# Optimization experiments

Hardware: AMD Instinct MI355X
Metric: run time of the kernel (lower is better)

The kernel has to match this reference:

```python
import jax, jax.numpy as jnp
import numpy as np

D_MODEL = 1024
NHEAD = 16
HEAD_DIM = D_MODEL // NHEAD
D_FF = 4096
EPS = 1e-5


def _layer_norm(x, g, b):
    mu = jnp.mean(x, axis=-1, keepdims=True)
    var = jnp.mean((x - mu) ** 2, axis=-1, keepdims=True)
    return (x - mu) * jax.lax.rsqrt(var + EPS) * g + b


def _rotate_every_two(x):
    x1 = x[..., ::2]
    x2 = x[..., 1::2]
    return jnp.stack([-x2, x1], axis=-1).reshape(x.shape)


def _rope_cos_sin(pos_start, length, head_dim, dtype):
    inv_freq = 1.0 / (10000.0 ** (jnp.arange(0, head_dim, 2, dtype=jnp.float32) / head_dim))
    pos = jnp.arange(pos_start, pos_start + length, dtype=jnp.float32)
    ang = jnp.einsum('i,j->ij', pos, inv_freq)  # (len, head_dim/2)
    cos = jnp.repeat(jnp.cos(ang), 2, axis=-1).astype(dtype)
    sin = jnp.repeat(jnp.sin(ang), 2, axis=-1).astype(dtype)
    return cos, sin


def setup_inputs() -> dict:
    key = jax.random.key(0)
    ks = jax.random.split(key, 16)
    s = 1.0 / np.sqrt(D_MODEL)
    sf = 1.0 / np.sqrt(D_FF)
    inp = {
        'src': jax.random.normal(ks[0], (2048, 2, D_MODEL), jnp.float32),
        'src_mask': jnp.ones((2048, 2048), jnp.float32),
        'Wq': jax.random.normal(ks[1], (D_MODEL, D_MODEL), jnp.float32) * s,
        'bq': jnp.zeros((D_MODEL,), jnp.float32),
        'Wk': jax.random.normal(ks[2], (D_MODEL, D_MODEL), jnp.float32) * s,
        'bk': jnp.zeros((D_MODEL,), jnp.float32),
        'Wv': jax.random.normal(ks[3], (D_MODEL, D_MODEL), jnp.float32) * s,
        'bv': jnp.zeros((D_MODEL,), jnp.float32),
        'Wo': jax.random.normal(ks[4], (D_MODEL, D_MODEL), jnp.float32) * s,
        'bo': jnp.zeros((D_MODEL,), jnp.float32),
        'W1': jax.random.normal(ks[5], (D_MODEL, D_FF), jnp.float32) * s,
        'b1': jnp.zeros((D_FF,), jnp.float32),
        'W2': jax.random.normal(ks[6], (D_FF, D_MODEL), jnp.float32) * sf,
        'b2': jnp.zeros((D_MODEL,), jnp.float32),
        'g1': jnp.ones((D_MODEL,), jnp.float32),
        'be1': jnp.zeros((D_MODEL,), jnp.float32),
        'g2': jnp.ones((D_MODEL,), jnp.float32),
        'be2': jnp.zeros((D_MODEL,), jnp.float32),
    }
    return inp


def _attention(q, k, v, attn_mask):
    # q, k, v: (S, B, D) already projected
    s, b, _ = q.shape
    kl = k.shape[0]

    def heads(x):
        # (L, B, D) -> (B, H, L, dh)
        return x.reshape(x.shape[0], b, NHEAD, HEAD_DIM).transpose(1, 2, 0, 3)

    qh, kh, vh = heads(q), heads(k), heads(v)
    q_cos, q_sin = _rope_cos_sin(0, s, HEAD_DIM, qh.dtype)
    k_cos, k_sin = _rope_cos_sin(0, kl, HEAD_DIM, kh.dtype)
    qh = qh * q_cos + _rotate_every_two(qh) * q_sin
    kh = kh * k_cos + _rotate_every_two(kh) * k_sin

    scores = jnp.einsum('bhqd,bhkd->bhqk', qh, kh) / np.sqrt(HEAD_DIM)
    if attn_mask is not None:
        scores = jnp.where(attn_mask[None, None, :, :] < 0.1, -jnp.inf, scores)
    w = jax.nn.softmax(scores, axis=-1)
    out = jnp.einsum('bhqk,bhkd->bhqd', w, vh)  # (B, H, S, dh)
    out = out.transpose(2, 0, 1, 3).reshape(s, b, D_MODEL)
    return out


def reference(src, src_mask, Wq, bq, Wk, bk, Wv, bv, Wo, bo, W1, b1, W2, b2, g1, be1, g2, be2):
    q = src @ Wq + bq
    k = src @ Wk + bk
    v = src @ Wv + bv
    attn = _attention(q, k, v, src_mask) @ Wo + bo
    src2 = _layer_norm(src + attn, g1, be1)
    ff = jax.nn.relu(src2 @ W1 + b1) @ W2 + b2
    out = _layer_norm(src2 + ff, g2, be2)
    return out
```

## Files before the change

kernel.cpp:

```cpp
#include <hip/hip_runtime.h>
#include <math.h>

#define S_LEN 2048
#define DM 1024
#define NH 16
#define HD 64
#define DFF 4096
#define MROWS 4096

typedef unsigned short u16;
typedef __attribute__((ext_vector_type(8))) __bf16 bf16x8;
typedef __attribute__((ext_vector_type(4))) float f32x4;
typedef __attribute__((ext_vector_type(16))) float f32x16;
typedef __attribute__((ext_vector_type(4))) int int32x4;

__device__ __forceinline__ u16 f2bf(float f) {
  unsigned u = __float_as_uint(f);
  unsigned r = (u + 0x7fffu + ((u >> 16) & 1u)) >> 16;
  return (u16)r;
}

__device__ __forceinline__ float bf2f(u16 u) {
  return __uint_as_float((unsigned)u << 16);
}

__device__ __forceinline__ unsigned cvtpk_bf16(float lo, float hi) {
  unsigned r;
  asm("v_cvt_pk_bf16_f32 %0, %1, %2" : "=v"(r) : "v"(lo), "v"(hi));
  return r;
}

__device__ __forceinline__ void gload_lds16(const void* g, void* l) {
  __builtin_amdgcn_global_load_lds((__attribute__((address_space(1))) void*)g,
                                   (__attribute__((address_space(3))) void*)l, 16, 0, 0);
}

__global__ __launch_bounds__(256) void k_transpose4(const float* __restrict__ W0, const float* __restrict__ W1,
                                                    const float* __restrict__ W2, const float* __restrict__ W3,
                                                    u16* __restrict__ T0, u16* __restrict__ T1,
                                                    u16* __restrict__ T2, u16* __restrict__ T3) {
  __shared__ float tile[32][33];
  const float* W = blockIdx.z == 0 ? W0 : blockIdx.z == 1 ? W1 : blockIdx.z == 2 ? W2 : W3;
  u16* Wt = blockIdx.z == 0 ? T0 : blockIdx.z == 1 ? T1 : blockIdx.z == 2 ? T2 : T3;
  int n0 = blockIdx.x * 32, k0 = blockIdx.y * 32;
  int tx = threadIdx.x & 31, ty = threadIdx.x >> 5;
  #pragma unroll
  for (int r = ty; r < 32; r += 8) tile[r][tx] = W[(size_t)(k0 + r) * 1024 + n0 + tx];
  __syncthreads();
  #pragma unroll
  for (int r = ty; r < 32; r += 8) Wt[(size_t)(n0 + r) * 1024 + k0 + tx] = f2bf(tile[tx][r]);
}

__global__ __launch_bounds__(256) void k_transpose_bf16(const float* __restrict__ W,
                                                        u16* __restrict__ Wt, int K, int N) {
  __shared__ float tile[32][33];
  int n0 = blockIdx.x * 32, k0 = blockIdx.y * 32;
  int tx = threadIdx.x & 31, ty = threadIdx.x >> 5;
  #pragma unroll
  for (int r = ty; r < 32; r += 8) tile[r][tx] = W[(size_t)(k0 + r) * N + n0 + tx];
  __syncthreads();
  #pragma unroll
  for (int r = ty; r < 32; r += 8) Wt[(size_t)(n0 + r) * K + k0 + tx] = f2bf(tile[tx][r]);
}

__global__ __launch_bounds__(256) void k_f2bf4(const float4* __restrict__ in,
                                               ushort4* __restrict__ out, int n4) {
  int i = blockIdx.x * 256 + threadIdx.x;
  if (i >= n4) return;
  float4 v = in[i];
  ushort4 o;
  o.x = f2bf(v.x); o.y = f2bf(v.y); o.z = f2bf(v.z); o.w = f2bf(v.w);
  out[i] = o;
}

__global__ __launch_bounds__(256) void k_rope_table(float* __restrict__ cosT,
                                                    float* __restrict__ sinT) {
  int idx = blockIdx.x * 256 + threadIdx.x;
  if (idx >= S_LEN * 32) return;
  int s = idx >> 5, i = idx & 31;
  float inv = powf(10000.f, -(float)(2 * i) / 64.f);
  float ang = (float)s * inv;
  cosT[idx] = cosf(ang);
  sinT[idx] = sinf(ang);
}

__global__ __launch_bounds__(256) void k_cat3(const float* __restrict__ a, const float* __restrict__ b,
                                              const float* __restrict__ c, float* __restrict__ o) {
  int i = blockIdx.x * 256 + threadIdx.x;
  if (i >= 3072) return;
  o[i] = i < 1024 ? a[i] : (i < 2048 ? b[i - 1024] : c[i - 2048]);
}

__global__ __launch_bounds__(256) void k_mask_flags(const float* __restrict__ mask,
                                                    unsigned char* __restrict__ flags) {
  int kt = blockIdx.x, qt = blockIdx.y;
  const float* mp = mask + (size_t)(qt * 64) * S_LEN + kt * 64;
  int tr = threadIdx.x >> 2;
  int tc = (threadIdx.x & 3) * 16;
  int ok = 1;
  #pragma unroll
  for (int c = 0; c < 16; c += 4) {
    float4 v = *(const float4*)(mp + (size_t)tr * S_LEN + tc + c);
    ok &= (v.x >= 0.1f) & (v.y >= 0.1f) & (v.z >= 0.1f) & (v.w >= 0.1f);
  }
  ok = __all(ok) ? 1 : 0;
  __shared__ int sh[4];
  if ((threadIdx.x & 63) == 0) sh[threadIdx.x >> 6] = ok;
  __syncthreads();
  if (threadIdx.x == 0) flags[qt * 32 + kt] = (sh[0] & sh[1] & sh[2] & sh[3]) ? 0 : 1;
}

enum { EPI_F32 = 0, EPI_RELU_BF16 = 2, EPI_PARTB = 4, EPI_BF16 = 5 };

template <int EPI>
__global__ __launch_bounds__(512, 2) void k_gemm256(const u16* __restrict__ A,
                                                    const u16* __restrict__ Bt,
                                                    const float* __restrict__ bias,
                                                    float* __restrict__ Cf, u16* __restrict__ Cb,
                                                    int M, int N, int K, int ldc, int Kc) {
  __shared__ __attribute__((aligned(16))) u16 As[4][256 * 32];
  __shared__ __attribute__((aligned(16))) u16 Bs[4][256 * 32];

  int nx = gridDim.x;
  int nwg = nx * gridDim.y;
  int flat = blockIdx.y * nx + blockIdx.x;
  int id = (flat & 7) * (nwg >> 3) + (flat >> 3);
  int n0 = (id % nx) * 256;
  int m0 = (id / nx) * 256;
  int kz = blockIdx.z * Kc;

  int tid = threadIdx.x;
  int lane = tid & 63, w = tid >> 6;
  int wm = (w >> 2) * 128, wn = (w & 3) * 64;
  int l15 = lane & 15, l4 = lane >> 4;
  int NT = Kc >> 5;

  const u16* aS[2];
  const u16* bS[2];
  int dslot[2];
  #pragma unroll
  for (int j = 0; j < 2; ++j) {
    int P = j * 512 + tid;
    int r = P >> 2;
    int sl = (P & 3) ^ (r & 3);
    aS[j] = A + (size_t)(m0 + r) * K + kz + sl * 8;
    bS[j] = Bt + (size_t)(n0 + r) * K + kz + sl * 8;
    dslot[j] = j * 512 + w * 64;
  }

  f32x4 acc[8][4] = {};

  #pragma unroll
  for (int t = 0; t < 3; ++t) {
    #pragma unroll
    for (int j = 0; j < 2; ++j) {
      gload_lds16(aS[j] + t * 32, &As[t][dslot[j] * 8]);
      gload_lds16(bS[j] + t * 32, &Bs[t][dslot[j] * 8]);
    }
  }

  for (int t = 0; t < NT; ++t) {
    int buf = t & 3;
    if (t < NT - 2) asm volatile("s_waitcnt vmcnt(8)" ::: "memory");
    else if (t == NT - 2) asm volatile("s_waitcnt vmcnt(4)" ::: "memory");
    else asm volatile("s_waitcnt vmcnt(0)" ::: "memory");
    __builtin_amdgcn_s_barrier();

    if (t + 3 < NT) {
      int tn = t + 3;
      int bn = tn & 3;
      #pragma unroll
      for (int j = 0; j < 2; ++j) {
        gload_lds16(aS[j] + tn * 32, &As[bn][dslot[j] * 8]);
        gload_lds16(bS[j] + tn * 32, &Bs[bn][dslot[j] * 8]);
      }
    }

    bf16x8 af[8], bq[4];
    #pragma unroll
    for (int m = 0; m < 8; ++m) {
      int r = wm + m * 16 + l15;
      af[m] = *(const bf16x8*)&As[buf][r * 32 + (l4 ^ (r & 3)) * 8];
    }
    #pragma unroll
    for (int n = 0; n < 4; ++n) {
      int r = wn + n * 16 + l15;
      bq[n] = *(const bf16x8*)&Bs[buf][r * 32 + (l4 ^ (r & 3)) * 8];
    }
    __builtin_amdgcn_s_setprio(1);
    #pragma unroll
    for (int m = 0; m < 8; ++m)
      #pragma unroll
      for (int n = 0; n < 4; ++n)
        acc[m][n] = __builtin_amdgcn_mfma_f32_16x16x32_bf16(af[m], bq[n], acc[m][n], 0, 0, 0);
    __builtin_amdgcn_s_setprio(0);
  }

  size_t zoff = (size_t)blockIdx.z * M * ldc;
  #pragma unroll
  for (int m = 0; m < 8; ++m) {
    #pragma unroll
    for (int n = 0; n < 4; ++n) {
      int col = n0 + wn + n * 16 + l15;
      float bv = (EPI == EPI_PARTB) ? 0.f : bias[col];
      #pragma unroll
      for (int r = 0; r < 4; ++r) {
        int row = m0 + wm + m * 16 + l4 * 4 + r;
        float v = acc[m][n][r] + bv;
        size_t o = (size_t)row * ldc + col;
        if (EPI == EPI_F32) Cf[o] = v;
        else if (EPI == EPI_RELU_BF16) Cb[o] = f2bf(fmaxf(v, 0.f));
        else if (EPI == EPI_BF16) Cb[o] = f2bf(v);
        else Cb[zoff + o] = f2bf(v);
      }
    }
  }
}

#define QSCALE 0.180336881f
__global__ __launch_bounds__(256) void k_rope_heads(const u16* __restrict__ QKVb,
                                                    const float* __restrict__ cosT,
                                                    const float* __restrict__ sinT,
                                                    u16* __restrict__ Qh, u16* __restrict__ Kh,
                                                    u16* __restrict__ Vt) {
  int idx = blockIdx.x * 256 + threadIdx.x;
  if (idx >= MROWS * 512) return;
  int m = idx >> 9, c2 = idx & 511;
  int h = c2 >> 5, i = c2 & 31, d = 2 * i;
  int s = m >> 1, b = m & 1;
  int bh = b * NH + h;
  size_t base = (size_t)m * 3072 + h * 64 + d;
  float q0 = bf2f(QKVb[base]), q1 = bf2f(QKVb[base + 1]);
  float k0 = bf2f(QKVb[base + 1024]), k1 = bf2f(QKVb[base + 1025]);
  float v0 = bf2f(QKVb[base + 2048]), v1 = bf2f(QKVb[base + 2049]);
  float c = cosT[s * 32 + i], sn = sinT[s * 32 + i];
  size_t ho = ((size_t)bh * S_LEN + s) * 64 + d;
  Qh[ho]     = f2bf((q0 * c - q1 * sn) * QSCALE);
  Qh[ho + 1] = f2bf((q1 * c + q0 * sn) * QSCALE);
  Kh[ho]     = f2bf(k0 * c - k1 * sn);
  Kh[ho + 1] = f2bf(k1 * c + k0 * sn);
  size_t vo = ((size_t)bh * 64 + d) * S_LEN + s;
  Vt[vo] = f2bf(v0);
  Vt[vo + S_LEN] = f2bf(v1);
}

__global__ __launch_bounds__(256) void k_attn(const u16* __restrict__ Qh, const u16* __restrict__ Kh,
                                              const u16* __restrict__ Vt,
                                              const float* __restrict__ mask,
                                              const unsigned char* __restrict__ flags,
                                              u16* __restrict__ Out) {
  __shared__ __attribute__((aligned(16))) u16 Ks[2][128 * 64];
  __shared__ __attribute__((aligned(16))) u16 Vs[2][64 * 128];
  int f = blockIdx.y * gridDim.x + blockIdx.x;
  int xcd = f & 7, ii = f >> 3;
  int bh = xcd * 4 + (ii >> 4);
  int q0 = (ii & 15) * 128;
  int b = bh >> 4, h = bh & 15;
  int tid = threadIdx.x, lane = tid & 63, w = tid >> 6;
  int l31 = lane & 31, l5 = lane >> 5;

  int qrow = q0 + w * 32 + l31;
  int qt = qrow >> 6;

  bf16x8 qf[4];
  {
    const u16* qp = Qh + ((size_t)bh * S_LEN + qrow) * 64 + l5 * 8;
    #pragma unroll
    for (int dc = 0; dc < 4; ++dc) qf[dc] = *(const bf16x8*)(qp + dc * 16);
  }

  const u16* Kbase = Kh + (size_t)bh * S_LEN * 64;
  const u16* Vbase = Vt + (size_t)bh * 64 * S_LEN;

  int ksid[4], vsid[4];
  const u16* kg[4];
  const u16* vg[4];
  #pragma unroll
  for (int i = 0; i < 4; ++i) {
    int sid = i * 256 + tid;
    ksid[i] = sid;
    int kr = sid >> 3, kslot = sid & 7;
    kg[i] = Kbase + (size_t)kr * 64 + (kslot ^ (kr & 7)) * 8;
    vsid[i] = sid;
    int vr = sid >> 4, vslot = sid & 15;
    vg[i] = Vbase + (size_t)vr * S_LEN + ((vslot ^ (vr & 15))) * 8;
  }

  float m_run = -1e30f, l_run = 0.f;
  f32x16 oA = {}, oB = {};

  const int NTILE = S_LEN / 128;
  #pragma unroll
  for (int i = 0; i < 4; ++i) {
    gload_lds16(kg[i], &Ks[0][ksid[i] * 8]);
    gload_lds16(vg[i], &Vs[0][vsid[i] * 8]);
  }

  for (int t = 0; t < NTILE; ++t) {
    int cur = t & 1;
    int kv0 = t * 128;
    asm volatile("s_waitcnt vmcnt(0)" ::: "memory");
    __builtin_amdgcn_s_barrier();
    if (t + 1 < NTILE) {
      int kvn = (t + 1) * 128;
      #pragma unroll
      for (int i = 0; i < 4; ++i) {
        gload_lds16(kg[i] + (size_t)kvn * 64, &Ks[cur ^ 1][ksid[i] * 8]);
        gload_lds16(vg[i] + kvn, &Vs[cur ^ 1][vsid[i] * 8]);
      }
    }

    #pragma unroll
    for (int ksub = 0; ksub < 2; ++ksub) {
      int koff = ksub * 64;
      f32x16 sA = {}, sB = {};
      #pragma unroll
      for (int dc = 0; dc < 4; ++dc) {
        int r0 = koff + l31;
        int r1 = koff + 32 + l31;
        int slot = (dc * 2 + l5) ^ (l31 & 7);
        bf16x8 ka0 = *(const bf16x8*)&Ks[cur][r0 * 64 + slot * 8];
        bf16x8 ka1 = *(const bf16x8*)&Ks[cur][r1 * 64 + slot * 8];
        sA = __builtin_amdgcn_mfma_f32_32x32x16_bf16(ka0, qf[dc], sA, 0, 0, 0);
        sB = __builtin_amdgcn_mfma_f32_32x32x16_bf16(ka1, qf[dc], sB, 0, 0, 0);
      }

      int fl = flags[qt * 32 + ((kv0 + koff) >> 6)];
      if (fl) {
        const float* mrow = mask + (size_t)qrow * S_LEN + kv0 + koff;
        #pragma unroll
        for (int r = 0; r < 16; ++r) {
          int key = (r & 3) + 8 * (r >> 2) + 4 * l5;
          if (mrow[key] < 0.1f) sA[r] = -1e30f;
          if (mrow[key + 32] < 0.1f) sB[r] = -1e30f;
        }
      }

      float pm = m_run;
      #pragma unroll
      for (int r = 0; r < 16; ++r) pm = fmaxf(pm, fmaxf(sA[r], sB[r]));
      pm = fmaxf(pm, __shfl_xor(pm, 32, 64));
      if (!__all(pm <= m_run + 8.f)) {
        float corr = __builtin_amdgcn_exp2f(m_run - pm);
        m_run = pm;
        l_run *= corr;
        #pragma unroll
        for (int r = 0; r < 16; ++r) { oA[r] *= corr; oB[r] *= corr; }
      }
      float ps = 0.f;
      #pragma unroll
      for (int r = 0; r < 16; ++r) {
        sA[r] = __builtin_amdgcn_exp2f(sA[r] - m_run);
        sB[r] = __builtin_amdgcn_exp2f(sB[r] - m_run);
        ps += sA[r] + sB[r];
      }
      l_run += ps;

      #pragma unroll
      for (int kh = 0; kh < 2; ++kh) {
        f32x16 s = kh ? sB : sA;
        #pragma unroll
        for (int c = 0; c < 2; ++c) {
          int base = c * 8;
          unsigned u0 = cvtpk_bf16(s[base + 0], s[base + 1]);
          unsigned u1 = cvtpk_bf16(s[base + 2], s[base + 3]);
          unsigned u2 = cvtpk_bf16(s[base + 4], s[base + 5]);
          unsigned u3 = cvtpk_bf16(s[base + 6], s[base + 7]);
          asm volatile("v_permlane32_swap_b32 %0, %1" : "+v"(u0), "+v"(u2));
          asm volatile("v_permlane32_swap_b32 %0, %1" : "+v"(u1), "+v"(u3));
          int32x4 wds = {(int)u0, (int)u1, (int)u2, (int)u3};
          bf16x8 pb = *(bf16x8*)&wds;
          int kslot = ksub * 8 + (kh * 2 + c) * 2 + l5;
          int vr0 = l31, vr1 = 32 + l31;
          bf16x8 va0 = *(const bf16x8*)&Vs[cur][vr0 * 128 + (kslot ^ (vr0 & 15)) * 8];
          bf16x8 va1 = *(const bf16x8*)&Vs[cur][vr1 * 128 + (kslot ^ (vr1 & 15)) * 8];
          oA = __builtin_amdgcn_mfma_f32_32x32x16_bf16(va0, pb, oA, 0, 0, 0);
          oB = __builtin_amdgcn_mfma_f32_32x32x16_bf16(va1, pb, oB, 0, 0, 0);
        }
      }
    }
  }

  float l_tot = l_run + __shfl_xor(l_run, 32, 64);
  float inv = 1.f / l_tot;
  int mrow = qrow * 2 + b;
  u16* op = Out + (size_t)mrow * DM + h * 64;
  #pragma unroll
  for (int db = 0; db < 2; ++db) {
    f32x16 o = db ? oB : oA;
    #pragma unroll
    for (int g = 0; g < 4; ++g) {
      int d0 = db * 32 + 8 * g + 4 * l5;
      ushort4 st;
      st.x = f2bf(o[4 * g + 0] * inv);
      st.y = f2bf(o[4 * g + 1] * inv);
      st.z = f2bf(o[4 * g + 2] * inv);
      st.w = f2bf(o[4 * g + 3] * inv);
      *(ushort4*)(op + d0) = st;
    }
  }
}

__device__ __forceinline__ float wave_sum(float v) {
  #pragma unroll
  for (int off = 32; off >= 1; off >>= 1) v += __shfl_xor(v, off, 64);
  return v;
}

template <int WB>
__global__ __launch_bounds__(256) void k_lnp(const u16* __restrict__ pb, const float* __restrict__ addf,
                                             const float* __restrict__ bvec,
                                             const float* __restrict__ gw, const float* __restrict__ bw,
                                             float* __restrict__ Yf, u16* __restrict__ Yb) {
  int m = blockIdx.x;
  int tid = threadIdx.x, lane = tid & 63, w = tid >> 6;
  __shared__ float part[4];
  __shared__ float shv[2];
  float4 sc = ((const float4*)(addf + (size_t)m * DM))[tid];
  float4 bv = ((const float4*)bvec)[tid];
  float vx = sc.x + bv.x, vy = sc.y + bv.y, vz = sc.z + bv.z, vw = sc.w + bv.w;
  #pragma unroll
  for (int z = 0; z < 4; ++z) {
    ushort4 qv = ((const ushort4*)(pb + (size_t)z * MROWS * DM + (size_t)m * DM))[tid];
    vx += bf2f(qv.x); vy += bf2f(qv.y); vz += bf2f(qv.z); vw += bf2f(qv.w);
  }
  float s = wave_sum(vx + vy + vz + vw);
  if (lane == 0) part[w] = s;
  __syncthreads();
  if (tid == 0) shv[0] = (part[0] + part[1] + part[2] + part[3]) * (1.f / DM);
  __syncthreads();
  float mu = shv[0];
  float d0 = vx - mu, d1 = vy - mu, d2 = vz - mu, d3 = vw - mu;
  float q = wave_sum(d0 * d0 + d1 * d1 + d2 * d2 + d3 * d3);
  if (lane == 0) part[w] = q;
  __syncthreads();
  if (tid == 0) shv[1] = rsqrtf((part[0] + part[1] + part[2] + part[3]) * (1.f / DM) + 1e-5f);
  __syncthreads();
  float rstd = shv[1];
  float4 g4 = ((const float4*)gw)[tid];
  float4 b4 = ((const float4*)bw)[tid];
  float y0 = d0 * rstd * g4.x + b4.x;
  float y1 = d1 * rstd * g4.y + b4.y;
  float y2 = d2 * rstd * g4.z + b4.z;
  float y3 = d3 * rstd * g4.w + b4.w;
  ((float4*)(Yf + (size_t)m * DM))[tid] = make_float4(y0, y1, y2, y3);
  if (WB) {
    ushort4 o;
    o.x = f2bf(y0); o.y = f2bf(y1); o.z = f2bf(y2); o.w = f2bf(y3);
    ((ushort4*)(Yb + (size_t)m * DM))[tid] = o;
  }
}

extern "C" void kernel_launch(void* const* d_in, const int* in_sizes, int n_in,
                              void* d_out, int out_size, void* d_ws, size_t ws_size,
                              hipStream_t stream) {
  (void)in_sizes; (void)n_in; (void)out_size; (void)ws_size;
  const float* src  = (const float*)d_in[0];
  const float* mask = (const float*)d_in[1];
  const float* Wq = (const float*)d_in[2];  const float* bq  = (const float*)d_in[3];
  const float* Wk = (const float*)d_in[4];  const float* bk  = (const float*)d_in[5];
  const float* Wv = (const float*)d_in[6];  const float* bv  = (const float*)d_in[7];
  const float* Wo = (const float*)d_in[8];  const float* bo  = (const float*)d_in[9];
  const float* W1 = (const float*)d_in[10]; const float* b1  = (const float*)d_in[11];
  const float* W2 = (const float*)d_in[12]; const float* b2  = (const float*)d_in[13];
  const float* g1 = (const float*)d_in[14]; const float* be1 = (const float*)d_in[15];
  const float* g2 = (const float*)d_in[16]; const float* be2 = (const float*)d_in[17];
  float* out = (float*)d_out;

  char* base = (char*)d_ws;
  size_t off = 0;
  auto carve = [&](size_t bytes) -> void* {
    void* r = base + off;
    off += (bytes + 255) & ~(size_t)255;
    return r;
  };
  u16* Wq_t = (u16*)carve(2ull * 1024 * 1024);
  u16* Wk_t = (u16*)carve(2ull * 1024 * 1024);
  u16* Wv_t = (u16*)carve(2ull * 1024 * 1024);
  u16* Wo_t = (u16*)carve(2ull * 1024 * 1024);
  u16* W1_t = (u16*)carve(2ull * 4096 * 1024);
  u16* W2_t = (u16*)carve(2ull * 1024 * 4096);
  u16* Xbf  = (u16*)carve(2ull * 4096 * 1024);
  float* cosT = (float*)carve(4ull * 2048 * 32);
  float* sinT = (float*)carve(4ull * 2048 * 32);
  float* bqkv = (float*)carve(4ull * 3072);
  unsigned char* mflags = (unsigned char*)carve(1024);
  u16* attn_out = (u16*)carve(2ull * 4096 * 1024);
  float* src2f = (float*)carve(4ull * 4096 * 1024);
  float* QKV = (float*)carve(4ull * 4096 * 3072);
  u16* Qh = (u16*)carve(2ull * 32 * 2048 * 64);
  u16* Kh = (u16*)carve(2ull * 32 * 2048 * 64);
  u16* Vt = (u16*)carve(2ull * 32 * 2048 * 64);
  u16* QKVb = (u16*)QKV;
  u16* woPb = (u16*)QKV;
  u16* ff1 = (u16*)QKV;
  u16* ffPb = (u16*)((char*)QKV + 32ull * 1024 * 1024);
  u16* src2b = (u16*)Vt;

  dim3 blk(256);
  dim3 blk5(512);
  k_transpose4<<<dim3(32, 32, 4), blk, 0, stream>>>(Wq, Wk, Wv, Wo, Wq_t, Wk_t, Wv_t, Wo_t);
  k_transpose_bf16<<<dim3(128, 32), blk, 0, stream>>>(W1, W1_t, 1024, 4096);
  k_transpose_bf16<<<dim3(32, 128), blk, 0, stream>>>(W2, W2_t, 4096, 1024);
  k_f2bf4<<<dim3(4096), blk, 0, stream>>>((const float4*)src, (ushort4*)Xbf, 4096 * 1024 / 4);
  k_rope_table<<<dim3(256), blk, 0, stream>>>(cosT, sinT);
  k_cat3<<<dim3(12), blk, 0, stream>>>(bq, bk, bv, bqkv);
  k_mask_flags<<<dim3(32, 32), blk, 0, stream>>>(mask, mflags);
  k_gemm256<EPI_BF16><<<dim3(12, 16, 1), blk5, 0, stream>>>(Xbf, Wq_t, bqkv, nullptr, QKVb, 4096, 3072, 1024, 3072, 1024);
  k_rope_heads<<<dim3(MROWS * 512 / 256), blk, 0, stream>>>(QKVb, cosT, sinT, Qh, Kh, Vt);
  k_attn<<<dim3(16, 32), blk, 0, stream>>>(Qh, Kh, Vt, mask, mflags, attn_out);
  k_gemm256<EPI_PARTB><<<dim3(4, 16, 4), blk5, 0, stream>>>(attn_out, Wo_t, nullptr, nullptr, woPb, 4096, 1024, 1024, 1024, 256);
  k_lnp<1><<<dim3(4096), blk, 0, stream>>>(woPb, src, bo, g1, be1, src2f, src2b);
  k_gemm256<EPI_RELU_BF16><<<dim3(16, 16, 1), blk5, 0, stream>>>(src2b, W1_t, b1, nullptr, ff1, 4096, 4096, 1024, 4096, 1024);
  k_gemm256<EPI_PARTB><<<dim3(4, 16, 4), blk5, 0, stream>>>(ff1, W2_t, nullptr, nullptr, ffPb, 4096, 1024, 4096, 1024, 1024);
  k_lnp<0><<<dim3(4096), blk, 0, stream>>>(ffPb, src2f, b2, g2, be2, out, nullptr);
}
```

Baseline: 302.3 us.

## Merge prep launches, vectorize RoPE/V-transpose via LDS, add MFMA setprio

Folds the seven small preprocessing launches into two kernels (k_prep for the weight transposes and src conversion, k_misc for the RoPE table, bias concat and mask flags), cutting launch overhead. k_rope_heads is rewritten so each thread handles 16 contiguous elements with 128-bit loads and stores, and V is transposed through LDS so the Vt writes are coalesced instead of strided 2-byte stores. The attention kernel raises wave priority around its MFMA blocks with s_setprio. Risks: more branch and index arithmetic in the merged kernels, and the priority hints may not help scheduling.

Result: faster. 278.1 us (-8.0%).

```diff
diff --git a/kernel.cpp b/kernel.cpp
--- a/kernel.cpp
+++ b/kernel.cpp
@@ -35,65 +35,67 @@
                                    (__attribute__((address_space(3))) void*)l, 16, 0, 0);
 }
 
-__global__ __launch_bounds__(256) void k_transpose4(const float* __restrict__ W0, const float* __restrict__ W1,
-                                                    const float* __restrict__ W2, const float* __restrict__ W3,
-                                                    u16* __restrict__ T0, u16* __restrict__ T1,
-                                                    u16* __restrict__ T2, u16* __restrict__ T3) {
+__global__ __launch_bounds__(256) void k_prep(const float* __restrict__ Wq, const float* __restrict__ Wk,
+                                              const float* __restrict__ Wv, const float* __restrict__ Wo,
+                                              const float* __restrict__ W1, const float* __restrict__ W2,
+                                              u16* __restrict__ Wq_t, u16* __restrict__ Wk_t,
+                                              u16* __restrict__ Wv_t, u16* __restrict__ Wo_t,
+                                              u16* __restrict__ W1_t, u16* __restrict__ W2_t,
+                                              const float4* __restrict__ src4, ushort4* __restrict__ Xbf4) {
+  int flat = blockIdx.x;
+  if (flat >= 12288) {
+    int i = (flat - 12288) * 256 + threadIdx.x;
+    float4 v = src4[i];
+    ushort4 o;
+    o.x = f2bf(v.x); o.y = f2bf(v.y); o.z = f2bf(v.z); o.w = f2bf(v.w);
+    Xbf4[i] = o;
+    return;
+  }
   __shared__ float tile[32][33];
-  const float* W = blockIdx.z == 0 ? W0 : blockIdx.z == 1 ? W1 : blockIdx.z == 2 ? W2 : W3;
-  u16* Wt = blockIdx.z == 0 ? T0 : blockIdx.z == 1 ? T1 : blockIdx.z == 2 ? T2 : T3;
-  int n0 = blockIdx.x * 32, k0 = blockIdx.y * 32;
+  const float* W;
+  u16* Wt;
+  int local, nx, K, N;
+  if (flat < 4096) {
+    int z = flat >> 10;
+    W = z == 0 ? Wq : z == 1 ? Wk : z == 2 ? Wv : Wo;
+    Wt = z == 0 ? Wq_t : z == 1 ? Wk_t : z == 2 ? Wv_t : Wo_t;
+    local = flat & 1023; nx = 32; K = 1024; N = 1024;
+  } else if (flat < 8192) {
+    W = W1; Wt = W1_t; local = flat - 4096; nx = 128; K = 1024; N = 4096;
+  } else {
+    W = W2; Wt = W2_t; local = flat - 8192; nx = 32; K = 4096; N = 1024;
+  }
+  int n0 = (local % nx) * 32, k0 = (local / nx) * 32;
   int tx = threadIdx.x & 31, ty = threadIdx.x >> 5;
   #pragma unroll
-  for (int r = ty; r < 32; r += 8) tile[r][tx] = W[(size_t)(k0 + r) * 1024 + n0 + tx];
-  __syncthreads();
-  #pragma unroll
-  for (int r = ty; r < 32; r += 8) Wt[(size_t)(n0 + r) * 1024 + k0 + tx] = f2bf(tile[tx][r]);
-}
-
-__global__ __launch_bounds__(256) void k_transpose_bf16(const float* __restrict__ W,
-                                                        u16* __restrict__ Wt, int K, int N) {
-  __shared__ float tile[32][33];
-  int n0 = blockIdx.x * 32, k0 = blockIdx.y * 32;
-  int tx = threadIdx.x & 31, ty = threadIdx.x >> 5;
-  #pragma unroll
   for (int r = ty; r < 32; r += 8) tile[r][tx] = W[(size_t)(k0 + r) * N + n0 + tx];
   __syncthreads();
   #pragma unroll
   for (int r = ty; r < 32; r += 8) Wt[(size_t)(n0 + r) * K + k0 + tx] = f2bf(tile[tx][r]);
 }
 
-__global__ __launch_bounds__(256) void k_f2bf4(const float4* __restrict__ in,
-                                               ushort4* __restrict__ out, int n4) {
-  int i = blockIdx.x * 256 + threadIdx.x;
-  if (i >= n4) return;
-  float4 v = in[i];
-  ushort4 o;
-  o.x = f2bf(v.x); o.y = f2bf(v.y); o.z = f2bf(v.z); o.w = f2bf(v.w);
-  out[i] = o;
-}
-
-__global__ __launch_bounds__(256) void k_rope_table(float* __restrict__ cosT,
-                                                    float* __restrict__ sinT) {
-  int idx = blockIdx.x * 256 + threadIdx.x;
-  if (idx >= S_LEN * 32) return;
-  int s = idx >> 5, i = idx & 31;
-  float inv = powf(10000.f, -(float)(2 * i) / 64.f);
-  float ang = (float)s * inv;
-  cosT[idx] = cosf(ang);
-  sinT[idx] = sinf(ang);
-}
-
-__global__ __launch_bounds__(256) void k_cat3(const float* __restrict__ a, const float* __restrict__ b,
-                                              const float* __restrict__ c, float* __restrict__ o) {
-  int i = blockIdx.x * 256 + threadIdx.x;
-  if (i >= 3072) return;
-  o[i] = i < 1024 ? a[i] : (i < 2048 ? b[i - 1024] : c[i - 2048]);
-}
-
-__global__ __launch_bounds__(256) void k_mask_flags(const float* __restrict__ mask,
-                                                    unsigned char* __restrict__ flags) {
-  int kt = blockIdx.x, qt = blockIdx.y;
+__global__ __launch_bounds__(256) void k_misc(float* __restrict__ cosT, float* __restrict__ sinT,
+                                              const float* __restrict__ bq, const float* __restrict__ bk,
+                                              const float* __restrict__ bv, float* __restrict__ bqkv,
+                                              const float* __restrict__ mask,
+                                              unsigned char* __restrict__ flags) {
+  int flat = blockIdx.x;
+  if (flat < 256) {
+    int idx = flat * 256 + threadIdx.x;
+    int s = idx >> 5, i = idx & 31;
+    float inv = powf(10000.f, -(float)(2 * i) / 64.f);
+    float ang = (float)s * inv;
+    cosT[idx] = cosf(ang);
+    sinT[idx] = sinf(ang);
+    return;
+  }
+  if (flat < 268) {
+    int i = (flat - 256) * 256 + threadIdx.x;
+    if (i < 3072) bqkv[i] = i < 1024 ? bq[i] : (i < 2048 ? bk[i - 1024] : bv[i - 2048]);
+    return;
+  }
+  int local = flat - 268;
+  int kt = local & 31, qt = local >> 5;
   const float* mp = mask + (size_t)(qt * 64) * S_LEN + kt * 64;
   int tr = threadIdx.x >> 2;
   int tc = (threadIdx.x & 3) * 16;
@@ -223,25 +225,69 @@
                                                     const float* __restrict__ sinT,
                                                     u16* __restrict__ Qh, u16* __restrict__ Kh,
                                                     u16* __restrict__ Vt) {
-  int idx = blockIdx.x * 256 + threadIdx.x;
-  if (idx >= MROWS * 512) return;
-  int m = idx >> 9, c2 = idx & 511;
-  int h = c2 >> 5, i = c2 & 31, d = 2 * i;
-  int s = m >> 1, b = m & 1;
-  int bh = b * NH + h;
-  size_t base = (size_t)m * 3072 + h * 64 + d;
-  float q0 = bf2f(QKVb[base]), q1 = bf2f(QKVb[base + 1]);
-  float k0 = bf2f(QKVb[base + 1024]), k1 = bf2f(QKVb[base + 1025]);
-  float v0 = bf2f(QKVb[base + 2048]), v1 = bf2f(QKVb[base + 2049]);
-  float c = cosT[s * 32 + i], sn = sinT[s * 32 + i];
-  size_t ho = ((size_t)bh * S_LEN + s) * 64 + d;
-  Qh[ho]     = f2bf((q0 * c - q1 * sn) * QSCALE);
-  Qh[ho + 1] = f2bf((q1 * c + q0 * sn) * QSCALE);
-  Kh[ho]     = f2bf(k0 * c - k1 * sn);
-  Kh[ho + 1] = f2bf(k1 * c + k0 * sn);
-  size_t vo = ((size_t)bh * 64 + d) * S_LEN + s;
-  Vt[vo] = f2bf(v0);
-  Vt[vo + S_LEN] = f2bf(v1);
+  __shared__ u16 Vlds[64 * 80];
+  int bh = blockIdx.y;
+  int s0 = blockIdx.x * 64;
+  int b = bh >> 4, h = bh & 15;
+  int tid = threadIdx.x;
+  int sr = tid >> 2, dg = (tid & 3) * 16;
+  int s = s0 + sr;
+  size_t rowbase = (size_t)(s * 2 + b) * 3072 + h * 64 + dg;
+
+  float4 c0 = *(const float4*)&cosT[s * 32 + (dg >> 1)];
+  float4 c1 = *(const float4*)&cosT[s * 32 + (dg >> 1) + 4];
+  float4 sn0 = *(const float4*)&sinT[s * 32 + (dg >> 1)];
+  float4 sn1 = *(const float4*)&sinT[s * 32 + (dg >> 1) + 4];
+  float cs[8] = {c0.x, c0.y, c0.z, c0.w, c1.x, c1.y, c1.z, c1.w};
+  float sn[8] = {sn0.x, sn0.y, sn0.z, sn0.w, sn1.x, sn1.y, sn1.z, sn1.w};
+
+  {
+    uint4 a = *(const uint4*)&QKVb[rowbase];
+    uint4 bbu = *(const uint4*)&QKVb[rowbase + 8];
+    unsigned ws[8] = {a.x, a.y, a.z, a.w, bbu.x, bbu.y, bbu.z, bbu.w};
+    unsigned o[8];
+    #pragma unroll
+    for (int j = 0; j < 8; ++j) {
+      float lo = bf2f((u16)(ws[j] & 0xffff)), hi = bf2f((u16)(ws[j] >> 16));
+      o[j] = cvtpk_bf16((lo * cs[j] - hi * sn[j]) * QSCALE, (hi * cs[j] + lo * sn[j]) * QSCALE);
+    }
+    u16* qp = &Qh[((size_t)bh * S_LEN + s) * 64 + dg];
+    *(uint4*)qp = (uint4){o[0], o[1], o[2], o[3]};
+    *(uint4*)(qp + 8) = (uint4){o[4], o[5], o[6], o[7]};
+  }
+  {
+    uint4 a = *(const uint4*)&QKVb[rowbase + 1024];
+    uint4 bbu = *(const uint4*)&QKVb[rowbase + 1032];
+    unsigned ws[8] = {a.x, a.y, a.z, a.w, bbu.x, bbu.y, bbu.z, bbu.w};
+    unsigned o[8];
+    #pragma unroll
+    for (int j = 0; j < 8; ++j) {
+      float lo = bf2f((u16)(ws[j] & 0xffff)), hi = bf2f((u16)(ws[j] >> 16));
+      o[j] = cvtpk_bf16(lo * cs[j] - hi * sn[j], hi * cs[j] + lo * sn[j]);
+    }
+    u16* kp = &Kh[((size_t)bh * S_LEN + s) * 64 + dg];
+    *(uint4*)kp = (uint4){o[0], o[1], o[2], o[3]};
+    *(uint4*)(kp + 8) = (uint4){o[4], o[5], o[6], o[7]};
+  }
+  {
+    uint4 a = *(const uint4*)&QKVb[rowbase + 2048];
+    uint4 bbu = *(const uint4*)&QKVb[rowbase + 2056];
+    unsigned ws[8] = {a.x, a.y, a.z, a.w, bbu.x, bbu.y, bbu.z, bbu.w};
+    #pragma unroll
+    for (int j = 0; j < 8; ++j) {
+      Vlds[(dg + 2 * j) * 80 + sr] = (u16)(ws[j] & 0xffff);
+      Vlds[(dg + 2 * j + 1) * 80 + sr] = (u16)(ws[j] >> 16);
+    }
+  }
+  __syncthreads();
+  {
+    int d = tid >> 2, sg = (tid & 3) * 16;
+    uint4 v0 = *(const uint4*)&Vlds[d * 80 + sg];
+    uint4 v1 = *(const uint4*)&Vlds[d * 80 + sg + 8];
+    u16* vp = &Vt[((size_t)bh * 64 + d) * S_LEN + s0 + sg];
+    *(uint4*)vp = v0;
+    *(uint4*)(vp + 8) = v1;
+  }
 }
 
 __global__ __launch_bounds__(256) void k_attn(const u16* __restrict__ Qh, const u16* __restrict__ Kh,
@@ -314,6 +360,7 @@
     for (int ksub = 0; ksub < 2; ++ksub) {
       int koff = ksub * 64;
       f32x16 sA = {}, sB = {};
+      __builtin_amdgcn_s_setprio(1);
       #pragma unroll
       for (int dc = 0; dc < 4; ++dc) {
         int r0 = koff + l31;
@@ -324,6 +371,7 @@
         sA = __builtin_amdgcn_mfma_f32_32x32x16_bf16(ka0, qf[dc], sA, 0, 0, 0);
         sB = __builtin_amdgcn_mfma_f32_32x32x16_bf16(ka1, qf[dc], sB, 0, 0, 0);
       }
+      __builtin_amdgcn_s_setprio(0);
 
       int fl = flags[qt * 32 + ((kv0 + koff) >> 6)];
       if (fl) {
@@ -356,6 +404,7 @@
       }
       l_run += ps;
 
+      __builtin_amdgcn_s_setprio(1);
       #pragma unroll
       for (int kh = 0; kh < 2; ++kh) {
         f32x16 s = kh ? sB : sA;
@@ -378,6 +427,7 @@
           oB = __builtin_amdgcn_mfma_f32_32x32x16_bf16(va1, pb, oB, 0, 0, 0);
         }
       }
+      __builtin_amdgcn_s_setprio(0);
     }
   }
 
@@ -499,15 +549,11 @@
 
   dim3 blk(256);
   dim3 blk5(512);
-  k_transpose4<<<dim3(32, 32, 4), blk, 0, stream>>>(Wq, Wk, Wv, Wo, Wq_t, Wk_t, Wv_t, Wo_t);
-  k_transpose_bf16<<<dim3(128, 32), blk, 0, stream>>>(W1, W1_t, 1024, 4096);
-  k_transpose_bf16<<<dim3(32, 128), blk, 0, stream>>>(W2, W2_t, 4096, 1024);
-  k_f2bf4<<<dim3(4096), blk, 0, stream>>>((const float4*)src, (ushort4*)Xbf, 4096 * 1024 / 4);
-  k_rope_table<<<dim3(256), blk, 0, stream>>>(cosT, sinT);
-  k_cat3<<<dim3(12), blk, 0, stream>>>(bq, bk, bv, bqkv);
-  k_mask_flags<<<dim3(32, 32), blk, 0, stream>>>(mask, mflags);
+  k_prep<<<dim3(16384), blk, 0, stream>>>(Wq, Wk, Wv, Wo, W1, W2, Wq_t, Wk_t, Wv_t, Wo_t,
+                                          W1_t, W2_t, (const float4*)src, (ushort4*)Xbf);
+  k_misc<<<dim3(1292), blk, 0, stream>>>(cosT, sinT, bq, bk, bv, bqkv, mask, mflags);
   k_gemm256<EPI_BF16><<<dim3(12, 16, 1), blk5, 0, stream>>>(Xbf, Wq_t, bqkv, nullptr, QKVb, 4096, 3072, 1024, 3072, 1024);
-  k_rope_heads<<<dim3(MROWS * 512 / 256), blk, 0, stream>>>(QKVb, cosT, sinT, Qh, Kh, Vt);
+  k_rope_heads<<<dim3(32, 32), blk, 0, stream>>>(QKVb, cosT, sinT, Qh, Kh, Vt);
   k_attn<<<dim3(16, 32), blk, 0, stream>>>(Qh, Kh, Vt, mask, mflags, attn_out);
   k_gemm256<EPI_PARTB><<<dim3(4, 16, 4), blk5, 0, stream>>>(attn_out, Wo_t, nullptr, nullptr, woPb, 4096, 1024, 1024, 1024, 256);
   k_lnp<1><<<dim3(4096), blk, 0, stream>>>(woPb, src, bo, g1, be1, src2f, src2b);
```
